# Kernel optimization log

Measured on AMD Instinct MI355X. Metric: run time of the kernel, lower is better.

Reference implementation:

```python
import jax, jax.numpy as jnp
import numpy as np

N_NODES = 100000
N_EDGES = 600000
IN_FEAT = 128
HID = 128
N_CLASSES = 64


def setup_inputs() -> dict:
    key = jax.random.key(0)
    ks = jax.random.split(key, 24)
    inp = {}
    inp["x"] = jax.random.normal(ks[0], (N_NODES, IN_FEAT), dtype=jnp.float32)
    for i, r in enumerate(["r0", "r1"]):
        inp[f"src_{r}"] = jax.random.randint(ks[1 + 3 * i], (N_EDGES,), 0, N_NODES, dtype=jnp.int32)
        inp[f"dst_{r}"] = jax.random.randint(ks[2 + 3 * i], (N_EDGES,), 0, N_NODES, dtype=jnp.int32)
        inp[f"ew_{r}"] = jax.random.uniform(ks[3 + 3 * i], (N_EDGES,), dtype=jnp.float32)
    def glorot(k, shape):
        fan = (shape[0] + shape[1]) / 2.0
        return jax.random.normal(k, shape, dtype=jnp.float32) / jnp.sqrt(fan)
    j = 7
    for r in ["r0", "r1"]:
        inp[f"Ws0_{r}"] = glorot(ks[j], (IN_FEAT, HID)); j += 1
        inp[f"Wn0_{r}"] = glorot(ks[j], (IN_FEAT, HID)); j += 1
        inp[f"b0_{r}"] = jnp.zeros((HID,), jnp.float32)
        inp[f"Wp_{r}"] = glorot(ks[j], (HID, HID)); j += 1
        inp[f"bp_{r}"] = jnp.zeros((HID,), jnp.float32)
        inp[f"Ws1_{r}"] = glorot(ks[j], (HID, N_CLASSES)); j += 1
        inp[f"Wn1_{r}"] = glorot(ks[j], (HID, N_CLASSES)); j += 1
        inp[f"b1_{r}"] = jnp.zeros((N_CLASSES,), jnp.float32)
    return inp


def _mean_agg(feat, src, dst, ew, n_nodes):
    # edge-weighted messages, mean over in-edges (divide by in-degree as DGL does)
    msg = feat[src] * ew[:, None]                      # [E, d]
    s = jax.ops.segment_sum(msg, dst, num_segments=n_nodes)
    deg = jax.ops.segment_sum(jnp.ones_like(ew), dst, num_segments=n_nodes)
    return s / jnp.maximum(deg, 1.0)[:, None]


def _max_agg(feat, src, dst, ew, n_nodes):
    msg = feat[src] * ew[:, None]                      # [E, d]
    m = jax.ops.segment_max(msg, dst, num_segments=n_nodes)
    deg = jax.ops.segment_sum(jnp.ones_like(ew), dst, num_segments=n_nodes)
    return jnp.where(deg[:, None] > 0, m, 0.0)         # zero for isolated nodes


def reference(x, src_r0, dst_r0, ew_r0, src_r1, dst_r1, ew_r1,
              Ws0_r0, Wn0_r0, b0_r0, Ws0_r1, Wn0_r1, b0_r1,
              Wp_r0, bp_r0, Ws1_r0, Wn1_r0, b1_r0,
              Wp_r1, bp_r1, Ws1_r1, Wn1_r1, b1_r1):
    n = x.shape[0]
    # Layer 0: per-relation SAGEConv(mean), HeteroGraphConv aggregate='sum', then relu
    h = jnp.zeros((n, Wn0_r0.shape[1]), x.dtype)
    for src, dst, ew, Ws, Wn, b in [
        (src_r0, dst_r0, ew_r0, Ws0_r0, Wn0_r0, b0_r0),
        (src_r1, dst_r1, ew_r1, Ws0_r1, Wn0_r1, b0_r1),
    ]:
        agg = _mean_agg(x, src, dst, ew, n)
        h = h + x @ Ws + agg @ Wn + b
    h = jax.nn.relu(h)
    # Classifier layer: per-relation SAGEConv(pool): relu(fc_pool(h_src)) -> max-agg
    logits = jnp.zeros((n, Wn1_r0.shape[1]), x.dtype)
    for src, dst, ew, Wp, bp, Ws, Wn, b in [
        (src_r0, dst_r0, ew_r0, Wp_r0, bp_r0, Ws1_r0, Wn1_r0, b1_r0),
        (src_r1, dst_r1, ew_r1, Wp_r1, bp_r1, Ws1_r1, Wn1_r1, b1_r1),
    ]:
        hp = jax.nn.relu(h @ Wp + bp)
        agg = _max_agg(hp, src, dst, ew, n)
        logits = logits + h @ Ws + agg @ Wn + b
    return logits
```

## Files before the change

kernel.cpp:

```cpp
#include <hip/hip_runtime.h>

typedef short bf16x8 __attribute__((ext_vector_type(8)));
typedef float f32x4 __attribute__((ext_vector_type(4)));
typedef float f32x2 __attribute__((ext_vector_type(2)));
typedef unsigned short u16;
typedef unsigned int u32;
typedef unsigned char u8;

#define NN 100000
#define NE 600000
#define PART 12500
#define ECH 4688

__device__ __forceinline__ u16 f2b(float f) {
    u32 u = __float_as_uint(f);
    return (u16)((u + 0x7FFFu + ((u >> 16) & 1u)) >> 16);
}

__global__ __launch_bounds__(256) void deg_part(
    const int* __restrict__ d0, const int* __restrict__ d1,
    int* __restrict__ g0, int* __restrict__ g1)
{
    int part = blockIdx.x & 7;
    int sub = blockIdx.x >> 3;
    int rel = sub & 1;
    int chunk = sub >> 1;
    const int lo = part * PART, hi = lo + PART;
    const int* d = rel ? d1 : d0;
    int* g = rel ? g1 : g0;
    const int e0 = chunk * ECH;
    const int e1 = min(e0 + ECH, NE);
    for (int e = e0 + threadIdx.x; e < e1; e += 256) {
        int dd = d[e];
        if (dd >= lo && dd < hi) atomicAdd(&g[dd], 1);
    }
}

__global__ void fused_setup(
    const float* __restrict__ x, u16* __restrict__ xo, u8* __restrict__ x8,
    const float* __restrict__ Ws0_0, const float* __restrict__ Ws0_1,
    const float* __restrict__ Wn0_0, const float* __restrict__ Wn0_1,
    const float* __restrict__ Wp_0,  const float* __restrict__ Wp_1,
    const float* __restrict__ Ws1_0, const float* __restrict__ Ws1_1,
    const float* __restrict__ Wn1_0, const float* __restrict__ Wn1_1,
    const float* __restrict__ b0_0, const float* __restrict__ b0_1,
    const float* __restrict__ b1_0, const float* __restrict__ b1_1,
    const float* __restrict__ bp_0, const float* __restrict__ bp_1,
    u16* __restrict__ w, float* __restrict__ bsum0, float* __restrict__ bsum1,
    float* __restrict__ bpc)
{
    int bb = blockIdx.x;
    if (bb < 12500) {
        int t = bb * 256 + threadIdx.x;
        const float4 v = reinterpret_cast<const float4*>(x)[t];
        ushort4 r; r.x = f2b(v.x); r.y = f2b(v.y); r.z = f2b(v.z); r.w = f2b(v.w);
        reinterpret_cast<ushort4*>(xo)[t] = r;
        u32 p = __builtin_amdgcn_cvt_pk_fp8_f32(v.x, v.y, 0, false);
        p = __builtin_amdgcn_cvt_pk_fp8_f32(v.z, v.w, p, true);
        reinterpret_cast<u32*>(x8)[t] = p;
    } else {
        int t = (bb - 12500) * 256 + threadIdx.x;
        if (t < 81920) {
            int m = t >> 14, u = t & 16383;
            int n = u >> 7, k = u & 127;
            float v;
            if (m == 0)      v = Ws0_0[k * 128 + n] + Ws0_1[k * 128 + n];
            else if (m == 1) v = Wn0_0[k * 128 + n];
            else if (m == 2) v = Wn0_1[k * 128 + n];
            else if (m == 3) v = Wp_0[k * 128 + n];
            else             v = Wp_1[k * 128 + n];
            w[t] = f2b(v);
        } else if (t < 106496) {
            int u = t - 81920;
            int m = u >> 13; u &= 8191;
            int n = u >> 7, k = u & 127;
            float v;
            if (m == 0)      v = Ws1_0[k * 64 + n] + Ws1_1[k * 64 + n];
            else if (m == 1) v = Wn1_0[k * 64 + n];
            else             v = Wn1_1[k * 64 + n];
            w[t] = f2b(v);
        } else if (t < 106624) {
            int i = t - 106496; bsum0[i] = b0_0[i] + b0_1[i];
        } else if (t < 106688) {
            int i = t - 106624; bsum1[i] = b1_0[i] + b1_1[i];
        } else if (t < 106944) {
            int i = t - 106688; bpc[i] = (i < 128) ? bp_0[i] : bp_1[i - 128];
        }
    }
}

__global__ void scan_local(const int* __restrict__ deg0, const int* __restrict__ deg1,
                           int* __restrict__ offs0, int* __restrict__ offs1,
                           int* __restrict__ bsA, int* __restrict__ bsB)
{
    __shared__ int sm[1024];
    int rel = blockIdx.x >= 98;
    int blk = blockIdx.x - rel * 98;
    const int* in = rel ? deg1 : deg0;
    int* out = rel ? offs1 : offs0;
    int* bsum = rel ? bsB : bsA;
    int t = threadIdx.x;
    int i = blk * 1024 + t;
    int v = (i < NN) ? in[i] : 0;
    sm[t] = v;
    __syncthreads();
    for (int off = 1; off < 1024; off <<= 1) {
        int add = (t >= off) ? sm[t - off] : 0;
        __syncthreads();
        sm[t] += add;
        __syncthreads();
    }
    if (i < NN) out[i] = sm[t] - v;
    if (t == 1023) bsum[blk] = sm[1023];
}

__global__ void scan_bsums(int* __restrict__ bsA, int* __restrict__ bsB)
{
    __shared__ int sm[128];
    int* bsum = blockIdx.x ? bsB : bsA;
    int t = threadIdx.x;
    int v = (t < 98) ? bsum[t] : 0;
    sm[t] = v;
    __syncthreads();
    for (int off = 1; off < 128; off <<= 1) {
        int add = (t >= off) ? sm[t - off] : 0;
        __syncthreads();
        sm[t] += add;
        __syncthreads();
    }
    if (t < 98) bsum[t] = sm[t] - v;
}

__global__ void scan_add(int* __restrict__ offs0, int* __restrict__ offs1,
                         const int* __restrict__ bsA, const int* __restrict__ bsB,
                         int* __restrict__ cur0, int* __restrict__ cur1,
                         u32* __restrict__ csr0, u32* __restrict__ csr1)
{
    int rel = blockIdx.x >= 392;
    int i = (blockIdx.x - rel * 392) * 256 + threadIdx.x;
    int* offs = rel ? offs1 : offs0;
    int* cur = rel ? cur1 : cur0;
    const int* bsum = rel ? bsB : bsA;
    if (i < NN) {
        int v = offs[i] + bsum[i >> 10];
        offs[i] = v;
        cur[i] = v;
    }
    if (i == 0) offs[NN] = NE;
    if (blockIdx.x == 0 && threadIdx.x < 8) {
        csr0[NE + threadIdx.x] = 0;
        csr1[NE + threadIdx.x] = 0;
    }
}

__global__ __launch_bounds__(256) void build_csr_part(
    const int* __restrict__ src0, const int* __restrict__ dst0,
    const float* __restrict__ ew0,
    const int* __restrict__ src1, const int* __restrict__ dst1,
    const float* __restrict__ ew1,
    int* __restrict__ cur0, int* __restrict__ cur1,
    u32* __restrict__ csr0, u32* __restrict__ csr1)
{
    int part = blockIdx.x & 7;
    int sub = blockIdx.x >> 3;
    int rel = sub & 1;
    int chunk = sub >> 1;
    const int lo = part * PART, hi = lo + PART;
    const int* src = rel ? src1 : src0;
    const int* dst = rel ? dst1 : dst0;
    const float* ew = rel ? ew1 : ew0;
    int* cur = rel ? cur1 : cur0;
    u32* csr = rel ? csr1 : csr0;
    const int e0 = chunk * ECH;
    const int e1 = min(e0 + ECH, NE);
    for (int e = e0 + threadIdx.x; e < e1; e += 256) {
        int d = dst[e];
        if (d >= lo && d < hi) {
            int p = atomicAdd(&cur[d], 1);
            u32 q = (__float_as_uint(ew[e]) + 0x10000u) >> 17;
            csr[p] = ((u32)src[e] << 15) | q;
        }
    }
}

template<bool MAXAGG, bool FP8>
__global__ __launch_bounds__(256) void gather(
    const u8* __restrict__ F0, const u8* __restrict__ F1,
    const int* __restrict__ offs0, const u32* __restrict__ csr0, u16* __restrict__ o0,
    const int* __restrict__ offs1, const u32* __restrict__ csr1, u16* __restrict__ o1)
{
    int b = blockIdx.x;
    int rel = b >= 25000;
    const u8* F = rel ? F1 : F0;
    const int* offs = rel ? offs1 : offs0;
    const u32* csr = rel ? csr1 : csr0;
    u16* out = rel ? o1 : o0;
    int node = (b - rel * 25000) * 4 + (threadIdx.x >> 6);
    int lane2 = (threadIdx.x & 63) << 1;
    int beg = __builtin_amdgcn_readfirstlane(offs[node]);
    int end = __builtin_amdgcn_readfirstlane(offs[node + 1]);

    float a0 = 0.f, a1 = 0.f;
    for (int e = beg; e < end; e += 8) {
        u32 E[8], v[8];
#pragma unroll
        for (int i = 0; i < 8; ++i)
            E[i] = csr[e + i];
#pragma unroll
        for (int i = 0; i < 8; ++i) {
            if (FP8)
                v[i] = *reinterpret_cast<const u16*>(F + ((size_t)(E[i] >> 15) << 7) + lane2);
            else
                v[i] = *reinterpret_cast<const u32*>(F + ((size_t)(E[i] >> 15) << 8) + (lane2 << 1));
        }
#pragma unroll
        for (int i = 0; i < 8; ++i) {
            float wgt = (e + i < end) ? __uint_as_float(E[i] << 17) : 0.f;
            float f0, f1;
            if (FP8) {
                f32x2 d = __builtin_amdgcn_cvt_pk_f32_fp8(v[i], false);
                f0 = d.x; f1 = d.y;
            } else {
                f0 = __uint_as_float(v[i] << 16);
                f1 = __uint_as_float(v[i] & 0xFFFF0000u);
            }
            if (MAXAGG) { a0 = fmaxf(a0, f0 * wgt); a1 = fmaxf(a1, f1 * wgt); }
            else        { a0 = fmaf(f0, wgt, a0);   a1 = fmaf(f1, wgt, a1); }
        }
    }
    float s = MAXAGG ? 1.f : 1.f / fmaxf((float)(end - beg), 1.f);
    ushort2 r; r.x = f2b(a0 * s); r.y = f2b(a1 * s);
    *reinterpret_cast<ushort2*>(out + (size_t)node * 128 + lane2) = r;
}

template<int NPAIR, int COLGROUPS, int WAVES, bool RELU, bool OUTF32, bool DUAL>
__global__ __launch_bounds__(WAVES * 64, 2) void gemm_reg(
    const u16* __restrict__ A0, const u16* __restrict__ A1, const u16* __restrict__ A2,
    const u16* __restrict__ BT, const float* __restrict__ bias,
    float* __restrict__ outF, u16* __restrict__ outB, u16* __restrict__ outB2)
{
    constexpr int NC = COLGROUPS * 32;
    constexpr int RT = WAVES / COLGROUPS;
    constexpr int OST = DUAL ? (NC / 2) : NC;
    constexpr int NTILES = NN / 32;
    const int w = threadIdx.x >> 6, l = threadIdx.x & 63;
    const int cg = w % COLGROUPS, rsub = w / COLGROUPS;
    const int l15 = l & 15, lk = (l >> 4) << 3, rq = (l >> 4) << 2;

    bf16x8 bfr[NPAIR][4][2];
#pragma unroll
    for (int p = 0; p < NPAIR; ++p)
#pragma unroll
        for (int ks = 0; ks < 4; ++ks)
#pragma unroll
            for (int cf = 0; cf < 2; ++cf) {
                int n = p * NC + cg * 32 + cf * 16 + l15;
                bfr[p][ks][cf] = *reinterpret_cast<const bf16x8*>(BT + (size_t)n * 128 + ks * 32 + lk);
            }

    const u16* As[3] = {A0, A1, A2};
    const float bv0 = bias[cg * 32 + l15];
    const float bv1 = bias[cg * 32 + 16 + l15];

    for (int tile = blockIdx.x * RT + rsub; tile < NTILES; tile += gridDim.x * RT) {
        const size_t rowbase = (size_t)tile * 32;

        bf16x8 af[NPAIR][4][2];
#pragma unroll
        for (int p = 0; p < NPAIR; ++p) {
            const u16* A = As[p] + rowbase * 128;
#pragma unroll
            for (int ks = 0; ks < 4; ++ks) {
                const int k0 = ks * 32 + lk;
                af[p][ks][0] = *reinterpret_cast<const bf16x8*>(A + (size_t)l15 * 128 + k0);
                af[p][ks][1] = *reinterpret_cast<const bf16x8*>(A + (size_t)(16 + l15) * 128 + k0);
            }
        }

        f32x4 acc[2][2];
#pragma unroll
        for (int rf = 0; rf < 2; ++rf)
#pragma unroll
            for (int cf = 0; cf < 2; ++cf)
                acc[rf][cf] = f32x4{0.f, 0.f, 0.f, 0.f};

#pragma unroll
        for (int p = 0; p < NPAIR; ++p)
#pragma unroll
            for (int ks = 0; ks < 4; ++ks) {
                acc[0][0] = __builtin_amdgcn_mfma_f32_16x16x32_bf16(af[p][ks][0], bfr[p][ks][0], acc[0][0], 0, 0, 0);
                acc[0][1] = __builtin_amdgcn_mfma_f32_16x16x32_bf16(af[p][ks][0], bfr[p][ks][1], acc[0][1], 0, 0, 0);
                acc[1][0] = __builtin_amdgcn_mfma_f32_16x16x32_bf16(af[p][ks][1], bfr[p][ks][0], acc[1][0], 0, 0, 0);
                acc[1][1] = __builtin_amdgcn_mfma_f32_16x16x32_bf16(af[p][ks][1], bfr[p][ks][1], acc[1][1], 0, 0, 0);
            }

        u16* ob = outB;
        if (DUAL && cg >= 4) ob = outB2;
        const int colbase = (DUAL ? (cg & 3) : cg) * 32;
#pragma unroll
        for (int cf = 0; cf < 2; ++cf) {
            const int col = colbase + cf * 16 + l15;
            const float bv = cf ? bv1 : bv0;
#pragma unroll
            for (int rf = 0; rf < 2; ++rf) {
#pragma unroll
                for (int j = 0; j < 4; ++j) {
                    const size_t row = rowbase + rf * 16 + rq + j;
                    float v = acc[rf][cf][j] + bv;
                    if (RELU) v = fmaxf(v, 0.f);
                    if (OUTF32) outF[row * OST + col] = v;
                    else        ob[row * OST + col] = f2b(v);
                }
            }
        }
    }
}

extern "C" void kernel_launch(void* const* d_in, const int* in_sizes, int n_in,
                              void* d_out, int out_size, void* d_ws, size_t ws_size,
                              hipStream_t stream)
{
    const float* x     = (const float*)d_in[0];
    const int*   src0  = (const int*)d_in[1];
    const int*   dst0  = (const int*)d_in[2];
    const float* ew0   = (const float*)d_in[3];
    const int*   src1  = (const int*)d_in[4];
    const int*   dst1  = (const int*)d_in[5];
    const float* ew1   = (const float*)d_in[6];
    const float* Ws0_0 = (const float*)d_in[7];
    const float* Wn0_0 = (const float*)d_in[8];
    const float* b0_0  = (const float*)d_in[9];
    const float* Wp_0  = (const float*)d_in[10];
    const float* bp_0  = (const float*)d_in[11];
    const float* Ws1_0 = (const float*)d_in[12];
    const float* Wn1_0 = (const float*)d_in[13];
    const float* b1_0  = (const float*)d_in[14];
    const float* Ws0_1 = (const float*)d_in[15];
    const float* Wn0_1 = (const float*)d_in[16];
    const float* b0_1  = (const float*)d_in[17];
    const float* Wp_1  = (const float*)d_in[18];
    const float* bp_1  = (const float*)d_in[19];
    const float* Ws1_1 = (const float*)d_in[20];
    const float* Wn1_1 = (const float*)d_in[21];
    const float* b1_1  = (const float*)d_in[22];

    char* ws = (char*)d_ws;
    u16*   x16   = (u16*)(ws + 0);
    u16*   h16   = (u16*)(ws + 25600000);
    u16*   a0    = (u16*)(ws + 51200000);
    u16*   a1    = (u16*)(ws + 76800000);
    u16*   hp1   = (u16*)(ws + 102400000);
    u32*   csr0  = (u32*)(ws + 128000000);
    u32*   csr1  = (u32*)(ws + 130400032);
    int*   offs0 = (int*)(ws + 132800064);
    int*   offs1 = (int*)(ws + 133200080);
    int*   cur0  = (int*)(ws + 133600096);
    int*   cur1  = (int*)(ws + 134000096);
    int*   deg0  = (int*)(ws + 134400096);
    int*   deg1  = (int*)(ws + 134800096);
    int*   bsA   = (int*)(ws + 135200096);
    int*   bsB   = (int*)(ws + 135200608);
    u16*   wts   = (u16*)(ws + 135201120);
    float* bsum0 = (float*)(ws + 135414112);
    float* bsum1 = (float*)(ws + 135414624);
    float* bpc   = (float*)(ws + 135415136);
    u8*    x8    = (u8*)(ws + 136000000);

    u16* hp0 = x16;

    hipMemsetAsync(deg0, 0, 800000, stream);
    deg_part<<<2048, 256, 0, stream>>>(dst0, dst1, deg0, deg1);
    fused_setup<<<12918, 256, 0, stream>>>(
        x, x16, x8, Ws0_0, Ws0_1, Wn0_0, Wn0_1, Wp_0, Wp_1,
        Ws1_0, Ws1_1, Wn1_0, Wn1_1, b0_0, b0_1, b1_0, b1_1, bp_0, bp_1,
        wts, bsum0, bsum1, bpc);

    scan_local<<<196, 1024, 0, stream>>>(deg0, deg1, offs0, offs1, bsA, bsB);
    scan_bsums<<<2, 128, 0, stream>>>(bsA, bsB);
    scan_add<<<784, 256, 0, stream>>>(offs0, offs1, bsA, bsB, cur0, cur1, csr0, csr1);
    build_csr_part<<<2048, 256, 0, stream>>>(
        src0, dst0, ew0, src1, dst1, ew1, cur0, cur1, csr0, csr1);

    gather<false, true><<<50000, 256, 0, stream>>>(
        x8, x8, offs0, csr0, a0, offs1, csr1, a1);
    gemm_reg<3, 4, 4, true, false, false><<<1024, 256, 0, stream>>>(
        x16, a0, a1, wts, bsum0, nullptr, h16, nullptr);

    gemm_reg<1, 8, 8, true, false, true><<<512, 512, 0, stream>>>(
        h16, nullptr, nullptr, wts + 49152, bpc, nullptr, hp0, hp1);
    gather<true, false><<<50000, 256, 0, stream>>>(
        (const u8*)hp0, (const u8*)hp1, offs0, csr0, a0, offs1, csr1, a1);
    gemm_reg<3, 2, 4, false, true, false><<<782, 256, 0, stream>>>(
        h16, a0, a1, wts + 81920, bsum1, (float*)d_out, nullptr, nullptr);
}
```

Before: 362.3 us.

## Bucket edges by destination partition and stage GEMM A tiles through LDS

Edge preprocessing changes from re-scanning all edges once per destination partition (for both degree counting and CSR placement) to a single bucketing pass. That pass writes packed (src|weight, dst) entries into per-partition staging slots, and the degree and placement kernels then read only their own partition's entries. Separately, the register-only GEMMs become a double-buffered LDS kernel that prefetches the next 32-row tile with XOR-swizzled shared stores, so waves within a block share A loads and overlap loads with MFMA compute. Grid sizes are retuned to 768 blocks. The costs are an extra staging buffer written into workspace aliased with h16, more kernel launches, and extra barriers per tile.

```diff
diff --git a/kernel.cpp b/kernel.cpp
--- a/kernel.cpp
+++ b/kernel.cpp
@@ -10,29 +10,78 @@
 #define NN 100000
 #define NE 600000
 #define PART 12500
-#define ECH 4688
+#define NB 250
+#define CA 2400
 
 __device__ __forceinline__ u16 f2b(float f) {
     u32 u = __float_as_uint(f);
     return (u16)((u + 0x7FFFu + ((u >> 16) & 1u)) >> 16);
 }
 
-__global__ __launch_bounds__(256) void deg_part(
-    const int* __restrict__ d0, const int* __restrict__ d1,
+__global__ __launch_bounds__(256) void bucket_edges(
+    const int* __restrict__ src0, const int* __restrict__ dst0,
+    const float* __restrict__ ew0,
+    const int* __restrict__ src1, const int* __restrict__ dst1,
+    const float* __restrict__ ew1,
+    uint2* __restrict__ stg, int* __restrict__ cnt)
+{
+    int rel = blockIdx.x >= NB;
+    int b = blockIdx.x - rel * NB;
+    const int* src = rel ? src1 : src0;
+    const int* dst = rel ? dst1 : dst0;
+    const float* ew = rel ? ew1 : ew0;
+    __shared__ int lcur[8];
+    if (threadIdx.x < 8) lcur[threadIdx.x] = 0;
+    __syncthreads();
+    uint2* base = stg + (size_t)((rel * NB + b) * 8) * CA;
+    const int e0 = b * CA;
+    for (int e = e0 + threadIdx.x; e < e0 + CA; e += 256) {
+        int d = dst[e];
+        int part = d / PART;
+        u32 q = (__float_as_uint(ew[e]) + 0x10000u) >> 17;
+        u32 lo = ((u32)src[e] << 15) | q;
+        int pos = atomicAdd(&lcur[part], 1);
+        base[part * CA + pos] = make_uint2(lo, (u32)d);
+    }
+    __syncthreads();
+    if (threadIdx.x < 8)
+        cnt[(rel * NB + b) * 8 + threadIdx.x] = lcur[threadIdx.x];
+}
+
+__global__ __launch_bounds__(256) void deg_from_stg(
+    const uint2* __restrict__ stg, const int* __restrict__ cnt,
     int* __restrict__ g0, int* __restrict__ g1)
 {
     int part = blockIdx.x & 7;
     int sub = blockIdx.x >> 3;
-    int rel = sub & 1;
-    int chunk = sub >> 1;
-    const int lo = part * PART, hi = lo + PART;
-    const int* d = rel ? d1 : d0;
+    int rel = sub & 1, idx = sub >> 1;
     int* g = rel ? g1 : g0;
-    const int e0 = chunk * ECH;
-    const int e1 = min(e0 + ECH, NE);
-    for (int e = e0 + threadIdx.x; e < e1; e += 256) {
-        int dd = d[e];
-        if (dd >= lo && dd < hi) atomicAdd(&g[dd], 1);
+    for (int ab = idx * 2; ab < min(idx * 2 + 2, NB); ++ab) {
+        int n = cnt[(rel * NB + ab) * 8 + part];
+        const uint2* base = stg + (size_t)((rel * NB + ab) * 8 + part) * CA;
+        for (int i = threadIdx.x; i < n; i += 256)
+            atomicAdd(&g[base[i].y], 1);
+    }
+}
+
+__global__ __launch_bounds__(256) void place_csr(
+    const uint2* __restrict__ stg, const int* __restrict__ cnt,
+    int* __restrict__ cur0, int* __restrict__ cur1,
+    u32* __restrict__ csr0, u32* __restrict__ csr1)
+{
+    int part = blockIdx.x & 7;
+    int sub = blockIdx.x >> 3;
+    int rel = sub & 1, idx = sub >> 1;
+    int* cur = rel ? cur1 : cur0;
+    u32* csr = rel ? csr1 : csr0;
+    for (int ab = idx * 2; ab < min(idx * 2 + 2, NB); ++ab) {
+        int n = cnt[(rel * NB + ab) * 8 + part];
+        const uint2* base = stg + (size_t)((rel * NB + ab) * 8 + part) * CA;
+        for (int i = threadIdx.x; i < n; i += 256) {
+            uint2 en = base[i];
+            int p = atomicAdd(&cur[en.y], 1);
+            csr[p] = en.x;
+        }
     }
 }
 
@@ -153,36 +202,6 @@
     }
 }
 
-__global__ __launch_bounds__(256) void build_csr_part(
-    const int* __restrict__ src0, const int* __restrict__ dst0,
-    const float* __restrict__ ew0,
-    const int* __restrict__ src1, const int* __restrict__ dst1,
-    const float* __restrict__ ew1,
-    int* __restrict__ cur0, int* __restrict__ cur1,
-    u32* __restrict__ csr0, u32* __restrict__ csr1)
-{
-    int part = blockIdx.x & 7;
-    int sub = blockIdx.x >> 3;
-    int rel = sub & 1;
-    int chunk = sub >> 1;
-    const int lo = part * PART, hi = lo + PART;
-    const int* src = rel ? src1 : src0;
-    const int* dst = rel ? dst1 : dst0;
-    const float* ew = rel ? ew1 : ew0;
-    int* cur = rel ? cur1 : cur0;
-    u32* csr = rel ? csr1 : csr0;
-    const int e0 = chunk * ECH;
-    const int e1 = min(e0 + ECH, NE);
-    for (int e = e0 + threadIdx.x; e < e1; e += 256) {
-        int d = dst[e];
-        if (d >= lo && d < hi) {
-            int p = atomicAdd(&cur[d], 1);
-            u32 q = (__float_as_uint(ew[e]) + 0x10000u) >> 17;
-            csr[p] = ((u32)src[e] << 15) | q;
-        }
-    }
-}
-
 template<bool MAXAGG, bool FP8>
 __global__ __launch_bounds__(256) void gather(
     const u8* __restrict__ F0, const u8* __restrict__ F1,
@@ -234,18 +253,35 @@
 }
 
 template<int NPAIR, int COLGROUPS, int WAVES, bool RELU, bool OUTF32, bool DUAL>
-__global__ __launch_bounds__(WAVES * 64, 2) void gemm_reg(
+__global__ __launch_bounds__(WAVES * 64) void gemm_lds(
     const u16* __restrict__ A0, const u16* __restrict__ A1, const u16* __restrict__ A2,
     const u16* __restrict__ BT, const float* __restrict__ bias,
     float* __restrict__ outF, u16* __restrict__ outB, u16* __restrict__ outB2)
 {
     constexpr int NC = COLGROUPS * 32;
-    constexpr int RT = WAVES / COLGROUPS;
     constexpr int OST = DUAL ? (NC / 2) : NC;
     constexpr int NTILES = NN / 32;
-    const int w = threadIdx.x >> 6, l = threadIdx.x & 63;
-    const int cg = w % COLGROUPS, rsub = w / COLGROUPS;
+    constexpr int THREADS = WAVES * 64;
+    constexpr int NLOAD = NPAIR * 512 / THREADS;
+    constexpr int RS = WAVES / COLGROUPS;
+    __shared__ char lds[2 * NPAIR * 8192];
+
+    const int t = threadIdx.x;
+    const int w = t >> 6, l = t & 63;
+    const int cg = w % COLGROUPS;
+    const int rsub = w / COLGROUPS;
     const int l15 = l & 15, lk = (l >> 4) << 3, rq = (l >> 4) << 2;
+
+    const u16* As[3] = {A0, A1, A2};
+
+    int goff[NLOAD], loff[NLOAD];
+#pragma unroll
+    for (int j = 0; j < NLOAD; ++j) {
+        const int p = (j * THREADS) >> 9;
+        const int s = ((j * THREADS) & 511) + t;
+        goff[j] = s * 8;
+        loff[j] = p * 8192 + ((s * 16) ^ (((s >> 4) & 7) << 4));
+    }
 
     bf16x8 bfr[NPAIR][4][2];
 #pragma unroll
@@ -257,62 +293,89 @@
                 int n = p * NC + cg * 32 + cf * 16 + l15;
                 bfr[p][ks][cf] = *reinterpret_cast<const bf16x8*>(BT + (size_t)n * 128 + ks * 32 + lk);
             }
-
-    const u16* As[3] = {A0, A1, A2};
     const float bv0 = bias[cg * 32 + l15];
     const float bv1 = bias[cg * 32 + 16 + l15];
 
-    for (int tile = blockIdx.x * RT + rsub; tile < NTILES; tile += gridDim.x * RT) {
+    u16* ob = outB;
+    if (DUAL && cg >= 4) ob = outB2;
+    const int colbase = (DUAL ? (cg & 3) : cg) * 32;
+
+    uint4 v[NLOAD];
+    int tile = blockIdx.x;
+#pragma unroll
+    for (int j = 0; j < NLOAD; ++j) {
+        const int p = (j * THREADS) >> 9;
+        v[j] = *reinterpret_cast<const uint4*>(As[p] + (size_t)tile * 4096 + goff[j]);
+    }
+#pragma unroll
+    for (int j = 0; j < NLOAD; ++j)
+        *reinterpret_cast<uint4*>(&lds[loff[j]]) = v[j];
+    __syncthreads();
+
+    int buf = 0;
+    while (tile < NTILES) {
+        const int nxt = tile + (int)gridDim.x;
+        if (nxt < NTILES) {
+#pragma unroll
+            for (int j = 0; j < NLOAD; ++j) {
+                const int p = (j * THREADS) >> 9;
+                v[j] = *reinterpret_cast<const uint4*>(As[p] + (size_t)nxt * 4096 + goff[j]);
+            }
+        }
+
+        const int bb = buf * NPAIR * 8192;
+        f32x4 acc[2 / RS][2];
+#pragma unroll
+        for (int rr = 0; rr < 2 / RS; ++rr)
+#pragma unroll
+            for (int cf = 0; cf < 2; ++cf)
+                acc[rr][cf] = f32x4{0.f, 0.f, 0.f, 0.f};
+        const int sw = (l15 & 7) << 4;
+#pragma unroll
+        for (int p = 0; p < NPAIR; ++p) {
+            const int base = bb + p * 8192;
+#pragma unroll
+            for (int ks = 0; ks < 4; ++ks) {
+                const int cbyte = ks * 64 + lk * 2;
+#pragma unroll
+                for (int rr = 0; rr < 2 / RS; ++rr) {
+                    const int rf = (RS == 2) ? rsub : rr;
+                    bf16x8 a = *reinterpret_cast<const bf16x8*>(
+                        &lds[base + (((rf * 16 + l15) * 256 + cbyte) ^ sw)]);
+                    acc[rr][0] = __builtin_amdgcn_mfma_f32_16x16x32_bf16(a, bfr[p][ks][0], acc[rr][0], 0, 0, 0);
+                    acc[rr][1] = __builtin_amdgcn_mfma_f32_16x16x32_bf16(a, bfr[p][ks][1], acc[rr][1], 0, 0, 0);
+                }
+            }
+        }
+
         const size_t rowbase = (size_t)tile * 32;
-
-        bf16x8 af[NPAIR][4][2];
-#pragma unroll
-        for (int p = 0; p < NPAIR; ++p) {
-            const u16* A = As[p] + rowbase * 128;
-#pragma unroll
-            for (int ks = 0; ks < 4; ++ks) {
-                const int k0 = ks * 32 + lk;
-                af[p][ks][0] = *reinterpret_cast<const bf16x8*>(A + (size_t)l15 * 128 + k0);
-                af[p][ks][1] = *reinterpret_cast<const bf16x8*>(A + (size_t)(16 + l15) * 128 + k0);
-            }
-        }
-
-        f32x4 acc[2][2];
-#pragma unroll
-        for (int rf = 0; rf < 2; ++rf)
-#pragma unroll
-            for (int cf = 0; cf < 2; ++cf)
-                acc[rf][cf] = f32x4{0.f, 0.f, 0.f, 0.f};
-
-#pragma unroll
-        for (int p = 0; p < NPAIR; ++p)
-#pragma unroll
-            for (int ks = 0; ks < 4; ++ks) {
-                acc[0][0] = __builtin_amdgcn_mfma_f32_16x16x32_bf16(af[p][ks][0], bfr[p][ks][0], acc[0][0], 0, 0, 0);
-                acc[0][1] = __builtin_amdgcn_mfma_f32_16x16x32_bf16(af[p][ks][0], bfr[p][ks][1], acc[0][1], 0, 0, 0);
-                acc[1][0] = __builtin_amdgcn_mfma_f32_16x16x32_bf16(af[p][ks][1], bfr[p][ks][0], acc[1][0], 0, 0, 0);
-                acc[1][1] = __builtin_amdgcn_mfma_f32_16x16x32_bf16(af[p][ks][1], bfr[p][ks][1], acc[1][1], 0, 0, 0);
-            }
-
-        u16* ob = outB;
-        if (DUAL && cg >= 4) ob = outB2;
-        const int colbase = (DUAL ? (cg & 3) : cg) * 32;
 #pragma unroll
         for (int cf = 0; cf < 2; ++cf) {
             const int col = colbase + cf * 16 + l15;
             const float bv = cf ? bv1 : bv0;
 #pragma unroll
-            for (int rf = 0; rf < 2; ++rf) {
+            for (int rr = 0; rr < 2 / RS; ++rr) {
+                const int rf = (RS == 2) ? rsub : rr;
 #pragma unroll
                 for (int j = 0; j < 4; ++j) {
                     const size_t row = rowbase + rf * 16 + rq + j;
-                    float v = acc[rf][cf][j] + bv;
-                    if (RELU) v = fmaxf(v, 0.f);
-                    if (OUTF32) outF[row * OST + col] = v;
-                    else        ob[row * OST + col] = f2b(v);
+                    float vv = acc[rr][cf][j] + bv;
+                    if (RELU) vv = fmaxf(vv, 0.f);
+                    if (OUTF32) outF[row * OST + col] = vv;
+                    else        ob[row * OST + col] = f2b(vv);
                 }
             }
         }
+
+        if (nxt < NTILES) {
+            const int ob2 = (buf ^ 1) * NPAIR * 8192;
+#pragma unroll
+            for (int j = 0; j < NLOAD; ++j)
+                *reinterpret_cast<uint4*>(&lds[ob2 + loff[j]]) = v[j];
+        }
+        __syncthreads();
+        buf ^= 1;
+        tile = nxt;
     }
 }
 
@@ -350,6 +413,7 @@
     u16*   a0    = (u16*)(ws + 51200000);
     u16*   a1    = (u16*)(ws + 76800000);
     u16*   hp1   = (u16*)(ws + 102400000);
+    uint2* stg   = (uint2*)(ws + 25600000);
     u32*   csr0  = (u32*)(ws + 128000000);
     u32*   csr1  = (u32*)(ws + 130400032);
     int*   offs0 = (int*)(ws + 132800064);
@@ -364,32 +428,34 @@
     float* bsum0 = (float*)(ws + 135414112);
     float* bsum1 = (float*)(ws + 135414624);
     float* bpc   = (float*)(ws + 135415136);
+    int*   cnt   = (int*)(ws + 135416000);
     u8*    x8    = (u8*)(ws + 136000000);
 
     u16* hp0 = x16;
 
     hipMemsetAsync(deg0, 0, 800000, stream);
-    deg_part<<<2048, 256, 0, stream>>>(dst0, dst1, deg0, deg1);
+    bucket_edges<<<2 * NB, 256, 0, stream>>>(
+        src0, dst0, ew0, src1, dst1, ew1, stg, cnt);
+    deg_from_stg<<<2048, 256, 0, stream>>>(stg, cnt, deg0, deg1);
+    scan_local<<<196, 1024, 0, stream>>>(deg0, deg1, offs0, offs1, bsA, bsB);
+    scan_bsums<<<2, 128, 0, stream>>>(bsA, bsB);
+    scan_add<<<784, 256, 0, stream>>>(offs0, offs1, bsA, bsB, cur0, cur1, csr0, csr1);
+    place_csr<<<2048, 256, 0, stream>>>(stg, cnt, cur0, cur1, csr0, csr1);
+
     fused_setup<<<12918, 256, 0, stream>>>(
         x, x16, x8, Ws0_0, Ws0_1, Wn0_0, Wn0_1, Wp_0, Wp_1,
         Ws1_0, Ws1_1, Wn1_0, Wn1_1, b0_0, b0_1, b1_0, b1_1, bp_0, bp_1,
         wts, bsum0, bsum1, bpc);
 
-    scan_local<<<196, 1024, 0, stream>>>(deg0, deg1, offs0, offs1, bsA, bsB);
-    scan_bsums<<<2, 128, 0, stream>>>(bsA, bsB);
-    scan_add<<<784, 256, 0, stream>>>(offs0, offs1, bsA, bsB, cur0, cur1, csr0, csr1);
-    build_csr_part<<<2048, 256, 0, stream>>>(
-        src0, dst0, ew0, src1, dst1, ew1, cur0, cur1, csr0, csr1);
-
     gather<false, true><<<50000, 256, 0, stream>>>(
         x8, x8, offs0, csr0, a0, offs1, csr1, a1);
-    gemm_reg<3, 4, 4, true, false, false><<<1024, 256, 0, stream>>>(
+    gemm_lds<3, 4, 4, true, false, false><<<768, 256, 0, stream>>>(
         x16, a0, a1, wts, bsum0, nullptr, h16, nullptr);
 
-    gemm_reg<1, 8, 8, true, false, true><<<512, 512, 0, stream>>>(
+    gemm_lds<1, 8, 8, true, false, true><<<768, 512, 0, stream>>>(
         h16, nullptr, nullptr, wts + 49152, bpc, nullptr, hp0, hp1);
     gather<true, false><<<50000, 256, 0, stream>>>(
         (const u8*)hp0, (const u8*)hp1, offs0, csr0, a0, offs1, csr1, a1);
-    gemm_reg<3, 2, 4, false, true, false><<<782, 256, 0, stream>>>(
+    gemm_lds<3, 2, 4, false, true, false><<<768, 256, 0, stream>>>(
         h16, a0, a1, wts + 81920, bsum1, (float*)d_out, nullptr, nullptr);
 }
```

New measurement: 330.9 us. 8.6% less time.
